# Kernel optimization log

Hardware: AMD Instinct MI355X
Metric: run time of the kernel (lower is better)

## Reference

```python
import jax, jax.numpy as jnp
import numpy as np

N = 50000
E = 800000
D_IN = 128
D_H = 128
D_OUT = 40
BN_EPS = 1e-5


def setup_inputs() -> dict:
    key = jax.random.key(0)
    ks = jax.random.split(key, 16)
    s = lambda d: 1.0 / np.sqrt(d)
    inp = {
        "x": jax.random.normal(ks[0], (N, D_IN), jnp.float32),
        "edge_index": jax.random.randint(ks[1], (2, E), 0, N, jnp.int64),
        # conv1 MLP: Linear(D_IN,D_H) -> BN -> ReLU -> Linear(D_H,D_H) -> ReLU
        "W1a": jax.random.uniform(ks[2], (D_IN, D_H), jnp.float32, -s(D_IN), s(D_IN)),
        "b1a": jnp.zeros((D_H,), jnp.float32),
        "g1": jnp.ones((D_H,), jnp.float32),
        "be1": jnp.zeros((D_H,), jnp.float32),
        "W2a": jax.random.uniform(ks[3], (D_H, D_H), jnp.float32, -s(D_H), s(D_H)),
        "b2a": jnp.zeros((D_H,), jnp.float32),
        # conv2 MLP
        "W1b": jax.random.uniform(ks[4], (D_H, D_H), jnp.float32, -s(D_H), s(D_H)),
        "b1b": jnp.zeros((D_H,), jnp.float32),
        "g2": jnp.ones((D_H,), jnp.float32),
        "be2": jnp.zeros((D_H,), jnp.float32),
        "W2b": jax.random.uniform(ks[5], (D_H, D_H), jnp.float32, -s(D_H), s(D_H)),
        "b2b": jnp.zeros((D_H,), jnp.float32),
        # head
        "Wl1": jax.random.uniform(ks[6], (D_H, D_H), jnp.float32, -s(D_H), s(D_H)),
        "bl1": jnp.zeros((D_H,), jnp.float32),
        "Wl2": jax.random.uniform(ks[7], (D_H, D_OUT), jnp.float32, -s(D_H), s(D_H)),
        "bl2": jnp.zeros((D_OUT,), jnp.float32),
    }
    return inp


def _batchnorm(h, gamma, beta):
    # BatchNorm1d in training mode: biased batch stats over the node dim
    mu = h.mean(axis=0)
    var = h.var(axis=0)
    return (h - mu) * jax.lax.rsqrt(var + BN_EPS) * gamma + beta


def _gin_conv(x, src, dst, W1, b1, gamma, beta, W2, b2):
    # sum-aggregation over neighbors (eps = 0): (1+eps)*x + sum_{j in N(i)} x_j
    agg = x + jax.ops.segment_sum(x[src], dst, num_segments=N)
    h = agg @ W1 + b1
    h = jax.nn.relu(_batchnorm(h, gamma, beta))
    return jax.nn.relu(h @ W2 + b2)


def reference(x, edge_index, W1a, b1a, g1, be1, W2a, b2a,
              W1b, b1b, g2, be2, W2b, b2b, Wl1, bl1, Wl2, bl2):
    src, dst = edge_index[0], edge_index[1]
    h = jax.nn.relu(_gin_conv(x, src, dst, W1a, b1a, g1, be1, W2a, b2a))
    # dropout is a no-op here (deterministic reference / eval)
    h = _gin_conv(h, src, dst, W1b, b1b, g2, be2, W2b, b2b)
    h = jax.nn.relu(h @ Wl1 + bl1)
    h = h @ Wl2 + bl2
    return jax.nn.log_softmax(h, axis=1)
```

## Files before the change

### kernel.cpp

```cpp
#include <hip/hip_runtime.h>
#include <math.h>

#define NN 50000
#define NE 800000
#define DD 128
#define DOUT 40
#define BN_EPS_F 1e-5f
#define BSTRIDE 32
#define OVF_MAX 8192
#define NPX (NN / 8)
#define EPB 1024
#define BUCKET_BLOCKS (((NE + EPB - 1) / EPB) * 8)
#define X2BF_BLOCKS 6250
#define WPREP_BLOCKS ((5 * 16384 + 255) / 256)
#define NSLOT 8
#define HST 136

typedef __attribute__((ext_vector_type(8))) short bf16x8;
typedef __attribute__((ext_vector_type(4))) float f32x4;

static __device__ __forceinline__ unsigned short f2bf(float f) {
  unsigned u = __float_as_uint(f);
  unsigned r = (u + 0x7FFFu + ((u >> 16) & 1u)) >> 16;
  return (unsigned short)r;
}
static __device__ __forceinline__ float bf2f(unsigned short u) {
  return __uint_as_float((unsigned)u << 16);
}

__global__ void k_zero(int* __restrict__ cnt, float* __restrict__ stats,
                       int* __restrict__ ovfc) {
  int i = blockIdx.x * 256 + threadIdx.x;
  if (i < NN) cnt[i] = 0;
  if (i < 2 * NSLOT * 2 * DD) stats[i] = 0.f;
  if (i == 0) ovfc[0] = 0;
}

__global__ void k_bucketprep(const int* __restrict__ srcI, const int* __restrict__ dstI,
                             int* __restrict__ cnt, unsigned short* __restrict__ bkt,
                             int* __restrict__ ovfc, unsigned* __restrict__ ovf,
                             const float4* __restrict__ x, ushort4* __restrict__ xb,
                             const float* __restrict__ W0, const float* __restrict__ W1,
                             const float* __restrict__ W2, const float* __restrict__ W3,
                             const float* __restrict__ W4, unsigned short* __restrict__ wf) {
  int b = blockIdx.x;
  if (b < BUCKET_BLOCKS) {
    int xcd = b & 7;
    int chunk = b >> 3;
    int lo = xcd * NPX, hi = lo + NPX;
    int e0 = chunk * EPB + threadIdx.x * 4;
    if (e0 < NE) {
      int4 d4 = *(const int4*)(dstI + e0);
      int4 s4 = *(const int4*)(srcI + e0);
      int dd[4] = {d4.x, d4.y, d4.z, d4.w};
      int ss[4] = {s4.x, s4.y, s4.z, s4.w};
#pragma unroll
      for (int i = 0; i < 4; i++) {
        int d = dd[i];
        if (d >= lo && d < hi) {
          int r = atomicAdd(&cnt[d], 1);
          if (r < BSTRIDE) {
            bkt[(size_t)d * BSTRIDE + r] = (unsigned short)ss[i];
          } else {
            int o = atomicAdd(ovfc, 1);
            if (o < OVF_MAX) ovf[o] = ((unsigned)d << 16) | (unsigned)ss[i];
          }
        }
      }
    }
  } else if (b < BUCKET_BLOCKS + X2BF_BLOCKS) {
    int i = (b - BUCKET_BLOCKS) * 256 + threadIdx.x;
    if (i < NN * 32) {
      float4 v = x[i];
      ushort4 r;
      r.x = f2bf(v.x); r.y = f2bf(v.y); r.z = f2bf(v.z); r.w = f2bf(v.w);
      xb[i] = r;
    }
  } else {
    int fid = (b - BUCKET_BLOCKS - X2BF_BLOCKS) * 256 + threadIdx.x;
    if (fid >= 5 * 16384) return;
    int g = fid >> 14;
    int r = fid & 16383;
    int i = r & 7;
    int lane = (r >> 3) & 63;
    int ks = (r >> 9) & 3;
    int ct = r >> 11;
    int k = ks * 32 + (lane >> 4) * 8 + i;
    int col = ct * 16 + (lane & 15);
    const float* Wp = (g == 0) ? W0 : (g == 1) ? W1 : (g == 2) ? W2 : (g == 3) ? W3 : W4;
    float w = Wp[k * DD + col];
    wf[g * 16384 + r] = f2bf(w);
  }
}

__global__ __launch_bounds__(512) void k_aggemm(
    const unsigned short* __restrict__ in, const int* __restrict__ cnt,
    const unsigned short* __restrict__ bkt,
    const int* __restrict__ ovfc, const unsigned* __restrict__ ovf,
    const unsigned short* __restrict__ wf, const float* __restrict__ bias,
    unsigned short* __restrict__ outB, float* __restrict__ statsOut) {
  __shared__ __align__(16) short lw[16384];
  __shared__ __align__(16) unsigned short hs[64 * HST];
  __shared__ float lbias[DD], ls[DD], lq[DD];
  int tid = threadIdx.x;
  int lane = tid & 63, wv = tid >> 6;
  int rbase = blockIdx.x * 64;

  {
    const float4* src = (const float4*)wf;
    float4* dst = (float4*)lw;
#pragma unroll
    for (int it = 0; it < 4; it++) dst[it * 512 + tid] = src[it * 512 + tid];
  }
  if (tid < DD) { lbias[tid] = bias[tid]; ls[tid] = 0.f; lq[tid] = 0.f; }

  {
    int l16 = tid & 15;
    const unsigned short* base = in + l16 * 8;
#pragma unroll
    for (int rep = 0; rep < 2; rep++) {
      int nl = (tid >> 4) + rep * 32;
      int node = rbase + nl;
      float a[8] = {0.f, 0.f, 0.f, 0.f, 0.f, 0.f, 0.f, 0.f};
      if (node < NN) {
        bf16x8 sv = *(const bf16x8*)(base + (size_t)node * DD);
#pragma unroll
        for (int i = 0; i < 8; i++) a[i] = bf2f((unsigned short)sv[i]);
        int cn = cnt[node];
        int ce = (cn < BSTRIDE) ? cn : BSTRIDE;
        const unsigned short* bp = bkt + (size_t)node * BSTRIDE;
        int j = 0;
        for (; j + 3 < ce; j += 4) {
          int s0 = bp[j], s1 = bp[j + 1], s2 = bp[j + 2], s3 = bp[j + 3];
          bf16x8 v0 = *(const bf16x8*)(base + (size_t)s0 * DD);
          bf16x8 v1 = *(const bf16x8*)(base + (size_t)s1 * DD);
          bf16x8 v2 = *(const bf16x8*)(base + (size_t)s2 * DD);
          bf16x8 v3 = *(const bf16x8*)(base + (size_t)s3 * DD);
#pragma unroll
          for (int i = 0; i < 8; i++)
            a[i] += bf2f((unsigned short)v0[i]) + bf2f((unsigned short)v1[i]) +
                    bf2f((unsigned short)v2[i]) + bf2f((unsigned short)v3[i]);
        }
        for (; j < ce; j++) {
          bf16x8 v0 = *(const bf16x8*)(base + (size_t)bp[j] * DD);
#pragma unroll
          for (int i = 0; i < 8; i++) a[i] += bf2f((unsigned short)v0[i]);
        }
        if (cn > BSTRIDE) {
          int no = ovfc[0];
          if (no > OVF_MAX) no = OVF_MAX;
          for (int o = 0; o < no; o++) {
            unsigned pr = ovf[o];
            if ((int)(pr >> 16) == node) {
              bf16x8 v0 = *(const bf16x8*)(base + (size_t)(pr & 0xFFFFu) * DD);
#pragma unroll
              for (int i = 0; i < 8; i++) a[i] += bf2f((unsigned short)v0[i]);
            }
          }
        }
      }
      bf16x8 hv;
#pragma unroll
      for (int i = 0; i < 8; i++) hv[i] = (short)f2bf(a[i]);
      *(bf16x8*)(&hs[nl * HST + l16 * 8]) = hv;
    }
  }
  __syncthreads();

  int rblk = wv >> 1, ch = wv & 1;
  int kq = (lane >> 4) * 8;
  bf16x8 araw[4];
  {
    int lr = rblk * 16 + (lane & 15);
#pragma unroll
    for (int ks = 0; ks < 4; ks++)
      araw[ks] = *(const bf16x8*)(&hs[lr * HST + ks * 32 + kq]);
  }
  f32x4 acc[4];
#pragma unroll
  for (int ct = 0; ct < 4; ct++) acc[ct] = (f32x4){0.f, 0.f, 0.f, 0.f};
  const bf16x8* lwv = (const bf16x8*)lw;
#pragma unroll
  for (int ks = 0; ks < 4; ks++) {
#pragma unroll
    for (int ct = 0; ct < 4; ct++) {
      bf16x8 bh = lwv[((ch * 4 + ct) * 4 + ks) * 64 + lane];
      acc[ct] = __builtin_amdgcn_mfma_f32_16x16x32_bf16(araw[ks], bh, acc[ct], 0, 0, 0);
    }
  }

  {
    int r0 = rbase + rblk * 16 + (lane >> 4) * 4;
#pragma unroll
    for (int ct = 0; ct < 4; ct++) {
      int col = ch * 64 + ct * 16 + (lane & 15);
      float bb = lbias[col];
      float s = 0.f, q = 0.f;
#pragma unroll
      for (int j = 0; j < 4; j++) {
        int row = r0 + j;
        if (row < NN) {
          float v = acc[ct][j] + bb;
          outB[(size_t)row * DD + col] = f2bf(v);
          s += v; q += v * v;
        }
      }
      s += __shfl_xor(s, 16); s += __shfl_xor(s, 32);
      q += __shfl_xor(q, 16); q += __shfl_xor(q, 32);
      if ((lane >> 4) == 0) {
        atomicAdd(&ls[col], s);
        atomicAdd(&lq[col], q);
      }
    }
  }
  __syncthreads();
  if (tid < DD) {
    float* slot = statsOut + (blockIdx.x & (NSLOT - 1)) * 2 * DD;
    atomicAdd(&slot[tid], ls[tid]);
    atomicAdd(&slot[DD + tid], lq[tid]);
  }
}

template<bool BN_IN, bool RELU_OUT, bool STATS_OUT, bool HEAD>
__global__ __launch_bounds__(512) void k_mgemm(
    const unsigned short* __restrict__ in, const unsigned short* __restrict__ wf,
    const float* __restrict__ bias, float* __restrict__ outF,
    unsigned short* __restrict__ outB,
    const float* __restrict__ statsIn, float* __restrict__ statsOut,
    const float* __restrict__ gamma, const float* __restrict__ beta,
    const float* __restrict__ W2h, const float* __restrict__ b2h) {
  constexpr int SMEM_BYTES = HEAD ? 54272 : 32768;
  __shared__ __align__(16) char smem[SMEM_BYTES];
  __shared__ float scs[DD], shs[DD], lbias[DD], ls[DD], lq[DD];
  short* lw = (short*)smem;
  int tid = threadIdx.x;
  int lane = tid & 63, wv = tid >> 6;
  int rbase = blockIdx.x * 128 + wv * 16;
  int kq = (lane >> 4) * 8;

  bf16x8 araw[4];
  {
    int row = rbase + (lane & 15);
    bool v = row < NN;
    const unsigned short* ap = in + (size_t)row * DD + kq;
    bf16x8 zz = {0, 0, 0, 0, 0, 0, 0, 0};
#pragma unroll
    for (int ks = 0; ks < 4; ks++)
      araw[ks] = v ? *(const bf16x8*)(ap + ks * 32) : zz;
  }

  {
    const float4* src = (const float4*)wf;
    float4* dst = (float4*)lw;
#pragma unroll
    for (int it = 0; it < 4; it++) dst[it * 512 + tid] = src[it * 512 + tid];
  }
  if (tid < DD) {
    lbias[tid] = bias[tid];
    if (STATS_OUT) { ls[tid] = 0.f; lq[tid] = 0.f; }
    if (BN_IN) {
      float su = 0.f, sq = 0.f;
#pragma unroll
      for (int s = 0; s < NSLOT; s++) {
        su += statsIn[s * 2 * DD + tid];
        sq += statsIn[s * 2 * DD + DD + tid];
      }
      float mu  = su * (1.0f / NN);
      float var = sq * (1.0f / NN) - mu * mu;
      float sc  = gamma[tid] * rsqrtf(var + BN_EPS_F);
      scs[tid] = sc;
      shs[tid] = beta[tid] - mu * sc;
    }
  }
  __syncthreads();

  bf16x8 ahi[4];
  if constexpr (BN_IN) {
#pragma unroll
    for (int ks = 0; ks < 4; ks++) {
      const float4* s4 = (const float4*)&scs[ks * 32 + kq];
      const float4* h4 = (const float4*)&shs[ks * 32 + kq];
      float4 sa = s4[0], sb = s4[1], ha = h4[0], hb = h4[1];
      float ss[8] = {sa.x, sa.y, sa.z, sa.w, sb.x, sb.y, sb.z, sb.w};
      float hh[8] = {ha.x, ha.y, ha.z, ha.w, hb.x, hb.y, hb.z, hb.w};
      bf16x8 h;
#pragma unroll
      for (int i = 0; i < 8; i++) {
        float xv = fmaxf(bf2f((unsigned short)araw[ks][i]) * ss[i] + hh[i], 0.f);
        h[i] = (short)f2bf(xv);
      }
      ahi[ks] = h;
    }
  } else {
#pragma unroll
    for (int ks = 0; ks < 4; ks++) ahi[ks] = araw[ks];
  }

  f32x4 acc[8];
#pragma unroll
  for (int ct = 0; ct < 8; ct++) acc[ct] = (f32x4){0.f, 0.f, 0.f, 0.f};
  const bf16x8* lwv = (const bf16x8*)lw;
#pragma unroll
  for (int ks = 0; ks < 4; ks++) {
#pragma unroll
    for (int ct = 0; ct < 8; ct++) {
      bf16x8 bh = lwv[(ct * 4 + ks) * 64 + lane];
      acc[ct] = __builtin_amdgcn_mfma_f32_16x16x32_bf16(ahi[ks], bh, acc[ct], 0, 0, 0);
    }
  }

  if constexpr (!HEAD) {
    int r0 = rbase + (lane >> 4) * 4;
#pragma unroll
    for (int ct = 0; ct < 8; ct++) {
      int col = ct * 16 + (lane & 15);
      float bb = lbias[col];
      float s = 0.f, q = 0.f;
#pragma unroll
      for (int j = 0; j < 4; j++) {
        int row = r0 + j;
        if (row < NN) {
          float v = acc[ct][j] + bb;
          if (RELU_OUT) v = fmaxf(v, 0.f);
          outB[(size_t)row * DD + col] = f2bf(v);
          if (STATS_OUT) { s += v; q += v * v; }
        }
      }
      if (STATS_OUT) {
        s += __shfl_xor(s, 16); s += __shfl_xor(s, 32);
        q += __shfl_xor(q, 16); q += __shfl_xor(q, 32);
        if ((lane >> 4) == 0) {
          atomicAdd(&ls[col], s);
          atomicAdd(&lq[col], q);
        }
      }
    }
    if (STATS_OUT) {
      __syncthreads();
      if (tid < DD) {
        float* slot = statsOut + (blockIdx.x & (NSLOT - 1)) * 2 * DD;
        atomicAdd(&slot[tid], ls[tid]);
        atomicAdd(&slot[DD + tid], lq[tid]);
      }
    }
  } else {
    unsigned short* hs2 = (unsigned short*)smem;
    float* W2s = (float*)(smem + 33792);
    __syncthreads();
    {
      int lr0 = wv * 16 + (lane >> 4) * 4;
#pragma unroll
      for (int ct = 0; ct < 8; ct++) {
        int col = ct * 16 + (lane & 15);
        float bb = lbias[col];
#pragma unroll
        for (int j = 0; j < 4; j++) {
          float v = fmaxf(acc[ct][j] + bb, 0.f);
          hs2[(lr0 + j) * 132 + col] = f2bf(v);
        }
      }
      const float4* W2g = (const float4*)W2h;
      float4* W2s4 = (float4*)W2s;
#pragma unroll
      for (int it = 0; it < 3; it++) {
        int idx = it * 512 + tid;
        if (idx < 1280) W2s4[idx] = W2g[idx];
      }
    }
    __syncthreads();
    int lrow = tid >> 2, q = tid & 3;
    int grow = blockIdx.x * 128 + lrow;
    float a2[40];
#pragma unroll
    for (int j = 0; j < 40; j++) a2[j] = 0.f;
    for (int kk = 0; kk < 32; kk++) {
      int k = kk * 4 + q;
      float hv = bf2f(hs2[lrow * 132 + k]);
      const float4* wrow = (const float4*)(W2s + k * DOUT);
#pragma unroll
      for (int j4 = 0; j4 < 10; j4++) {
        float4 w = wrow[j4];
        a2[j4 * 4 + 0] += hv * w.x;
        a2[j4 * 4 + 1] += hv * w.y;
        a2[j4 * 4 + 2] += hv * w.z;
        a2[j4 * 4 + 3] += hv * w.w;
      }
    }
#pragma unroll
    for (int j = 0; j < 40; j++) {
      a2[j] += __shfl_xor(a2[j], 1);
      a2[j] += __shfl_xor(a2[j], 2);
    }
    if (q == 0 && grow < NN) {
      const float4* b24 = (const float4*)b2h;
      float m = -INFINITY;
#pragma unroll
      for (int j4 = 0; j4 < 10; j4++) {
        float4 bb = b24[j4];
        a2[j4 * 4 + 0] += bb.x; a2[j4 * 4 + 1] += bb.y;
        a2[j4 * 4 + 2] += bb.z; a2[j4 * 4 + 3] += bb.w;
      }
#pragma unroll
      for (int j = 0; j < 40; j++) m = fmaxf(m, a2[j]);
      float s = 0.f;
#pragma unroll
      for (int j = 0; j < 40; j++) s += expf(a2[j] - m);
      float d = m + logf(s);
      float4* out4 = (float4*)(outF + (size_t)grow * DOUT);
#pragma unroll
      for (int j4 = 0; j4 < 10; j4++) {
        float4 v = make_float4(a2[j4 * 4 + 0] - d, a2[j4 * 4 + 1] - d,
                               a2[j4 * 4 + 2] - d, a2[j4 * 4 + 3] - d);
        out4[j4] = v;
      }
    }
  }
}

extern "C" void kernel_launch(void* const* d_in, const int* in_sizes, int n_in,
                              void* d_out, int out_size, void* d_ws, size_t ws_size,
                              hipStream_t stream) {
  const float* x   = (const float*)d_in[0];
  const int*   ei  = (const int*)d_in[1];
  const float* W1a = (const float*)d_in[2];
  const float* b1a = (const float*)d_in[3];
  const float* g1  = (const float*)d_in[4];
  const float* be1 = (const float*)d_in[5];
  const float* W2a = (const float*)d_in[6];
  const float* b2a = (const float*)d_in[7];
  const float* W1b = (const float*)d_in[8];
  const float* b1b = (const float*)d_in[9];
  const float* g2  = (const float*)d_in[10];
  const float* be2 = (const float*)d_in[11];
  const float* W2b = (const float*)d_in[12];
  const float* b2b = (const float*)d_in[13];
  const float* Wl1 = (const float*)d_in[14];
  const float* bl1 = (const float*)d_in[15];
  const float* Wl2 = (const float*)d_in[16];
  const float* bl2 = (const float*)d_in[17];
  float* out = (float*)d_out;

  unsigned short* bufX = (unsigned short*)d_ws;
  unsigned short* bufA = bufX + (size_t)NN * DD;
  unsigned short* bufB = bufA + (size_t)NN * DD;
  float* stats1 = (float*)(bufB + (size_t)NN * DD);
  float* stats2 = stats1 + NSLOT * 2 * DD;
  int*   cnt    = (int*)(stats2 + NSLOT * 2 * DD);
  int*   ovfc   = cnt + NN;
  unsigned* ovf = (unsigned*)(ovfc + 4);
  unsigned short* bkt = (unsigned short*)(ovf + OVF_MAX);
  size_t wfOff = (((size_t)(bkt + (size_t)NN * BSTRIDE) - (size_t)d_ws) + 15) & ~(size_t)15;
  unsigned short* wfrag = (unsigned short*)((char*)d_ws + wfOff);

  const int* srcI = ei;
  const int* dstI = ei + NE;

  dim3 blk(256);
  int gemmGrid = (NN + 127) / 128;
  int agGrid   = (NN + 63) / 64;
  int bpGrid   = BUCKET_BLOCKS + X2BF_BLOCKS + WPREP_BLOCKS;
  int zeroGrid = (NN + 255) / 256;

  k_zero<<<zeroGrid, blk, 0, stream>>>(cnt, stats1, ovfc);
  k_bucketprep<<<bpGrid, blk, 0, stream>>>(srcI, dstI, cnt, bkt, ovfc, ovf,
                                           (const float4*)x, (ushort4*)bufX,
                                           W1a, W2a, W1b, W2b, Wl1, wfrag);

  k_aggemm<<<agGrid, 512, 0, stream>>>(bufX, cnt, bkt, ovfc, ovf,
                                       wfrag + 0 * 16384, b1a, bufB, stats1);
  k_mgemm<true, true, false, false><<<gemmGrid, 512, 0, stream>>>(
      bufB, wfrag + 1 * 16384, b2a, nullptr, bufA,
      stats1, nullptr, g1, be1, nullptr, nullptr);
  k_aggemm<<<agGrid, 512, 0, stream>>>(bufA, cnt, bkt, ovfc, ovf,
                                       wfrag + 2 * 16384, b1b, bufB, stats2);
  k_mgemm<true, true, false, false><<<gemmGrid, 512, 0, stream>>>(
      bufB, wfrag + 3 * 16384, b2b, nullptr, bufA,
      stats2, nullptr, g2, be2, nullptr, nullptr);
  k_mgemm<false, false, false, true><<<gemmGrid, 512, 0, stream>>>(
      bufA, wfrag + 4 * 16384, bl1, out, nullptr,
      nullptr, nullptr, nullptr, nullptr, Wl2, bl2);
}
```

Measured before the change: 192.4 us.

## Fuse second-conv output GEMM with head GEMMs into one tail kernel

Merges the conv2 second linear layer (BN+ReLU input, ReLU output) with the head Linear+ReLU+Linear+log_softmax into a single kernel. The intermediate activation stays in LDS (XOR-swizzled layout) instead of going to global memory, which removes one kernel launch and one full activation write/read. The non-head GEMM is specialized into a non-template kernel. The fused kernel uses more shared memory per block, which may reduce occupancy.

```diff
diff --git a/kernel.cpp b/kernel.cpp
--- a/kernel.cpp
+++ b/kernel.cpp
@@ -221,17 +221,13 @@
   }
 }
 
-template<bool BN_IN, bool RELU_OUT, bool STATS_OUT, bool HEAD>
-__global__ __launch_bounds__(512) void k_mgemm(
+__global__ __launch_bounds__(512) void k_mgemm2(
     const unsigned short* __restrict__ in, const unsigned short* __restrict__ wf,
-    const float* __restrict__ bias, float* __restrict__ outF,
-    unsigned short* __restrict__ outB,
-    const float* __restrict__ statsIn, float* __restrict__ statsOut,
-    const float* __restrict__ gamma, const float* __restrict__ beta,
-    const float* __restrict__ W2h, const float* __restrict__ b2h) {
-  constexpr int SMEM_BYTES = HEAD ? 54272 : 32768;
-  __shared__ __align__(16) char smem[SMEM_BYTES];
-  __shared__ float scs[DD], shs[DD], lbias[DD], ls[DD], lq[DD];
+    const float* __restrict__ bias, unsigned short* __restrict__ outB,
+    const float* __restrict__ statsIn,
+    const float* __restrict__ gamma, const float* __restrict__ beta) {
+  __shared__ __align__(16) char smem[32768];
+  __shared__ float scs[DD], shs[DD], lbias[DD];
   short* lw = (short*)smem;
   int tid = threadIdx.x;
   int lane = tid & 63, wv = tid >> 6;
@@ -248,7 +244,6 @@
     for (int ks = 0; ks < 4; ks++)
       araw[ks] = v ? *(const bf16x8*)(ap + ks * 32) : zz;
   }
-
   {
     const float4* src = (const float4*)wf;
     float4* dst = (float4*)lw;
@@ -257,43 +252,35 @@
   }
   if (tid < DD) {
     lbias[tid] = bias[tid];
-    if (STATS_OUT) { ls[tid] = 0.f; lq[tid] = 0.f; }
-    if (BN_IN) {
-      float su = 0.f, sq = 0.f;
-#pragma unroll
-      for (int s = 0; s < NSLOT; s++) {
-        su += statsIn[s * 2 * DD + tid];
-        sq += statsIn[s * 2 * DD + DD + tid];
-      }
-      float mu  = su * (1.0f / NN);
-      float var = sq * (1.0f / NN) - mu * mu;
-      float sc  = gamma[tid] * rsqrtf(var + BN_EPS_F);
-      scs[tid] = sc;
-      shs[tid] = beta[tid] - mu * sc;
-    }
+    float su = 0.f, sq = 0.f;
+#pragma unroll
+    for (int s = 0; s < NSLOT; s++) {
+      su += statsIn[s * 2 * DD + tid];
+      sq += statsIn[s * 2 * DD + DD + tid];
+    }
+    float mu  = su * (1.0f / NN);
+    float var = sq * (1.0f / NN) - mu * mu;
+    float sc  = gamma[tid] * rsqrtf(var + BN_EPS_F);
+    scs[tid] = sc;
+    shs[tid] = beta[tid] - mu * sc;
   }
   __syncthreads();
 
   bf16x8 ahi[4];
-  if constexpr (BN_IN) {
-#pragma unroll
-    for (int ks = 0; ks < 4; ks++) {
-      const float4* s4 = (const float4*)&scs[ks * 32 + kq];
-      const float4* h4 = (const float4*)&shs[ks * 32 + kq];
-      float4 sa = s4[0], sb = s4[1], ha = h4[0], hb = h4[1];
-      float ss[8] = {sa.x, sa.y, sa.z, sa.w, sb.x, sb.y, sb.z, sb.w};
-      float hh[8] = {ha.x, ha.y, ha.z, ha.w, hb.x, hb.y, hb.z, hb.w};
-      bf16x8 h;
-#pragma unroll
-      for (int i = 0; i < 8; i++) {
-        float xv = fmaxf(bf2f((unsigned short)araw[ks][i]) * ss[i] + hh[i], 0.f);
-        h[i] = (short)f2bf(xv);
-      }
-      ahi[ks] = h;
-    }
-  } else {
-#pragma unroll
-    for (int ks = 0; ks < 4; ks++) ahi[ks] = araw[ks];
+#pragma unroll
+  for (int ks = 0; ks < 4; ks++) {
+    const float4* s4 = (const float4*)&scs[ks * 32 + kq];
+    const float4* h4 = (const float4*)&shs[ks * 32 + kq];
+    float4 sa = s4[0], sb = s4[1], ha = h4[0], hb = h4[1];
+    float ss[8] = {sa.x, sa.y, sa.z, sa.w, sb.x, sb.y, sb.z, sb.w};
+    float hh[8] = {ha.x, ha.y, ha.z, ha.w, hb.x, hb.y, hb.z, hb.w};
+    bf16x8 h;
+#pragma unroll
+    for (int i = 0; i < 8; i++) {
+      float xv = fmaxf(bf2f((unsigned short)araw[ks][i]) * ss[i] + hh[i], 0.f);
+      h[i] = (short)f2bf(xv);
+    }
+    ahi[ks] = h;
   }
 
   f32x4 acc[8];
@@ -309,110 +296,222 @@
     }
   }
 
-  if constexpr (!HEAD) {
-    int r0 = rbase + (lane >> 4) * 4;
+  int r0 = rbase + (lane >> 4) * 4;
+#pragma unroll
+  for (int ct = 0; ct < 8; ct++) {
+    int col = ct * 16 + (lane & 15);
+    float bb = lbias[col];
+#pragma unroll
+    for (int j = 0; j < 4; j++) {
+      int row = r0 + j;
+      if (row < NN) {
+        float v = fmaxf(acc[ct][j] + bb, 0.f);
+        outB[(size_t)row * DD + col] = f2bf(v);
+      }
+    }
+  }
+}
+
+__global__ __launch_bounds__(512) void k_tail2(
+    const unsigned short* __restrict__ in, const unsigned short* __restrict__ wfA,
+    const float* __restrict__ biasA, const float* __restrict__ statsIn,
+    const float* __restrict__ gamma, const float* __restrict__ beta,
+    const unsigned short* __restrict__ wfB, const float* __restrict__ biasB,
+    const float* __restrict__ W2h, const float* __restrict__ b2h,
+    float* __restrict__ outF) {
+  __shared__ __align__(16) char R1[32768];
+  __shared__ __align__(16) char R2[32768];
+  __shared__ float scs[DD], shs[DD], lbA[DD], lbB[DD];
+  int tid = threadIdx.x;
+  int lane = tid & 63, wv = tid >> 6;
+  int rbase = blockIdx.x * 128 + wv * 16;
+  int kq = (lane >> 4) * 8;
+
+  bf16x8 araw[4];
+  {
+    int row = rbase + (lane & 15);
+    bool v = row < NN;
+    const unsigned short* ap = in + (size_t)row * DD + kq;
+    bf16x8 zz = {0, 0, 0, 0, 0, 0, 0, 0};
+#pragma unroll
+    for (int ks = 0; ks < 4; ks++)
+      araw[ks] = v ? *(const bf16x8*)(ap + ks * 32) : zz;
+  }
+  {
+    const float4* s1 = (const float4*)wfA;
+    const float4* s2 = (const float4*)wfB;
+    float4* d1 = (float4*)R1;
+    float4* d2 = (float4*)R2;
+#pragma unroll
+    for (int it = 0; it < 4; it++) {
+      d1[it * 512 + tid] = s1[it * 512 + tid];
+      d2[it * 512 + tid] = s2[it * 512 + tid];
+    }
+  }
+  if (tid < DD) {
+    lbA[tid] = biasA[tid];
+    lbB[tid] = biasB[tid];
+    float su = 0.f, sq = 0.f;
+#pragma unroll
+    for (int s = 0; s < NSLOT; s++) {
+      su += statsIn[s * 2 * DD + tid];
+      sq += statsIn[s * 2 * DD + DD + tid];
+    }
+    float mu  = su * (1.0f / NN);
+    float var = sq * (1.0f / NN) - mu * mu;
+    float sc  = gamma[tid] * rsqrtf(var + BN_EPS_F);
+    scs[tid] = sc;
+    shs[tid] = beta[tid] - mu * sc;
+  }
+  __syncthreads();
+
+  bf16x8 ahi[4];
+#pragma unroll
+  for (int ks = 0; ks < 4; ks++) {
+    const float4* s4 = (const float4*)&scs[ks * 32 + kq];
+    const float4* h4 = (const float4*)&shs[ks * 32 + kq];
+    float4 sa = s4[0], sb = s4[1], ha = h4[0], hb = h4[1];
+    float ss[8] = {sa.x, sa.y, sa.z, sa.w, sb.x, sb.y, sb.z, sb.w};
+    float hh[8] = {ha.x, ha.y, ha.z, ha.w, hb.x, hb.y, hb.z, hb.w};
+    bf16x8 h;
+#pragma unroll
+    for (int i = 0; i < 8; i++) {
+      float xv = fmaxf(bf2f((unsigned short)araw[ks][i]) * ss[i] + hh[i], 0.f);
+      h[i] = (short)f2bf(xv);
+    }
+    ahi[ks] = h;
+  }
+
+  f32x4 acc[8];
+#pragma unroll
+  for (int ct = 0; ct < 8; ct++) acc[ct] = (f32x4){0.f, 0.f, 0.f, 0.f};
+  {
+    const bf16x8* l1 = (const bf16x8*)R1;
+#pragma unroll
+    for (int ks = 0; ks < 4; ks++) {
+#pragma unroll
+      for (int ct = 0; ct < 8; ct++) {
+        bf16x8 bh = l1[(ct * 4 + ks) * 64 + lane];
+        acc[ct] = __builtin_amdgcn_mfma_f32_16x16x32_bf16(ahi[ks], bh, acc[ct], 0, 0, 0);
+      }
+    }
+  }
+  __syncthreads();
+
+  {
+    int fr0 = (lane >> 4) * 4;
+    int lr0 = wv * 16 + fr0;
 #pragma unroll
     for (int ct = 0; ct < 8; ct++) {
       int col = ct * 16 + (lane & 15);
-      float bb = lbias[col];
-      float s = 0.f, q = 0.f;
+      float bb = lbA[col];
 #pragma unroll
       for (int j = 0; j < 4; j++) {
-        int row = r0 + j;
-        if (row < NN) {
-          float v = acc[ct][j] + bb;
-          if (RELU_OUT) v = fmaxf(v, 0.f);
-          outB[(size_t)row * DD + col] = f2bf(v);
-          if (STATS_OUT) { s += v; q += v * v; }
-        }
-      }
-      if (STATS_OUT) {
-        s += __shfl_xor(s, 16); s += __shfl_xor(s, 32);
-        q += __shfl_xor(q, 16); q += __shfl_xor(q, 32);
-        if ((lane >> 4) == 0) {
-          atomicAdd(&ls[col], s);
-          atomicAdd(&lq[col], q);
-        }
-      }
-    }
-    if (STATS_OUT) {
-      __syncthreads();
-      if (tid < DD) {
-        float* slot = statsOut + (blockIdx.x & (NSLOT - 1)) * 2 * DD;
-        atomicAdd(&slot[tid], ls[tid]);
-        atomicAdd(&slot[DD + tid], lq[tid]);
-      }
-    }
-  } else {
-    unsigned short* hs2 = (unsigned short*)smem;
-    float* W2s = (float*)(smem + 33792);
-    __syncthreads();
-    {
-      int lr0 = wv * 16 + (lane >> 4) * 4;
+        int r = lr0 + j;
+        float v = fmaxf(acc[ct][j] + bb, 0.f);
+        int byt = (r * 256 + col * 2) ^ ((r & 7) << 4);
+        *(unsigned short*)(R1 + byt) = f2bf(v);
+      }
+    }
+  }
+  __syncthreads();
+
+  bf16x8 a2[4];
+  {
+    int lr = wv * 16 + (lane & 15);
+#pragma unroll
+    for (int ks = 0; ks < 4; ks++) {
+      int byt = (lr * 256 + ks * 64 + kq * 2) ^ ((lr & 7) << 4);
+      a2[ks] = *(const bf16x8*)(R1 + byt);
+    }
+  }
+  f32x4 ac3[8];
+#pragma unroll
+  for (int ct = 0; ct < 8; ct++) ac3[ct] = (f32x4){0.f, 0.f, 0.f, 0.f};
+  {
+    const bf16x8* l2 = (const bf16x8*)R2;
+#pragma unroll
+    for (int ks = 0; ks < 4; ks++) {
 #pragma unroll
       for (int ct = 0; ct < 8; ct++) {
-        int col = ct * 16 + (lane & 15);
-        float bb = lbias[col];
-#pragma unroll
-        for (int j = 0; j < 4; j++) {
-          float v = fmaxf(acc[ct][j] + bb, 0.f);
-          hs2[(lr0 + j) * 132 + col] = f2bf(v);
-        }
-      }
-      const float4* W2g = (const float4*)W2h;
-      float4* W2s4 = (float4*)W2s;
-#pragma unroll
-      for (int it = 0; it < 3; it++) {
-        int idx = it * 512 + tid;
-        if (idx < 1280) W2s4[idx] = W2g[idx];
-      }
-    }
-    __syncthreads();
-    int lrow = tid >> 2, q = tid & 3;
-    int grow = blockIdx.x * 128 + lrow;
-    float a2[40];
-#pragma unroll
-    for (int j = 0; j < 40; j++) a2[j] = 0.f;
-    for (int kk = 0; kk < 32; kk++) {
-      int k = kk * 4 + q;
-      float hv = bf2f(hs2[lrow * 132 + k]);
-      const float4* wrow = (const float4*)(W2s + k * DOUT);
-#pragma unroll
-      for (int j4 = 0; j4 < 10; j4++) {
-        float4 w = wrow[j4];
-        a2[j4 * 4 + 0] += hv * w.x;
-        a2[j4 * 4 + 1] += hv * w.y;
-        a2[j4 * 4 + 2] += hv * w.z;
-        a2[j4 * 4 + 3] += hv * w.w;
-      }
-    }
-#pragma unroll
-    for (int j = 0; j < 40; j++) {
-      a2[j] += __shfl_xor(a2[j], 1);
-      a2[j] += __shfl_xor(a2[j], 2);
-    }
-    if (q == 0 && grow < NN) {
-      const float4* b24 = (const float4*)b2h;
-      float m = -INFINITY;
-#pragma unroll
-      for (int j4 = 0; j4 < 10; j4++) {
-        float4 bb = b24[j4];
-        a2[j4 * 4 + 0] += bb.x; a2[j4 * 4 + 1] += bb.y;
-        a2[j4 * 4 + 2] += bb.z; a2[j4 * 4 + 3] += bb.w;
-      }
-#pragma unroll
-      for (int j = 0; j < 40; j++) m = fmaxf(m, a2[j]);
-      float s = 0.f;
-#pragma unroll
-      for (int j = 0; j < 40; j++) s += expf(a2[j] - m);
-      float d = m + logf(s);
-      float4* out4 = (float4*)(outF + (size_t)grow * DOUT);
-#pragma unroll
-      for (int j4 = 0; j4 < 10; j4++) {
-        float4 v = make_float4(a2[j4 * 4 + 0] - d, a2[j4 * 4 + 1] - d,
-                               a2[j4 * 4 + 2] - d, a2[j4 * 4 + 3] - d);
-        out4[j4] = v;
-      }
+        bf16x8 bh = l2[(ct * 4 + ks) * 64 + lane];
+        ac3[ct] = __builtin_amdgcn_mfma_f32_16x16x32_bf16(a2[ks], bh, ac3[ct], 0, 0, 0);
+      }
+    }
+  }
+  __syncthreads();
+
+  {
+    int fr0 = (lane >> 4) * 4;
+    int lr0 = wv * 16 + fr0;
+#pragma unroll
+    for (int ct = 0; ct < 8; ct++) {
+      int col = ct * 16 + (lane & 15);
+      float bb = lbB[col];
+#pragma unroll
+      for (int j = 0; j < 4; j++) {
+        int r = lr0 + j;
+        float v = fmaxf(ac3[ct][j] + bb, 0.f);
+        int byt = (r * 256 + col * 2) ^ ((r & 7) << 4);
+        *(unsigned short*)(R1 + byt) = f2bf(v);
+      }
+    }
+    const float4* W2g = (const float4*)W2h;
+    float4* W2s4 = (float4*)R2;
+#pragma unroll
+    for (int it = 0; it < 3; it++) {
+      int idx = it * 512 + tid;
+      if (idx < 1280) W2s4[idx] = W2g[idx];
+    }
+  }
+  __syncthreads();
+
+  int lrow = tid >> 2, q = tid & 3;
+  int grow = blockIdx.x * 128 + lrow;
+  const float* W2s = (const float*)R2;
+  float av[40];
+#pragma unroll
+  for (int j = 0; j < 40; j++) av[j] = 0.f;
+  for (int kk = 0; kk < 32; kk++) {
+    int k = kk * 4 + q;
+    int byt = (lrow * 256 + k * 2) ^ ((lrow & 7) << 4);
+    float hv = bf2f(*(const unsigned short*)(R1 + byt));
+    const float4* wrow = (const float4*)(W2s + k * DOUT);
+#pragma unroll
+    for (int j4 = 0; j4 < 10; j4++) {
+      float4 w = wrow[j4];
+      av[j4 * 4 + 0] += hv * w.x;
+      av[j4 * 4 + 1] += hv * w.y;
+      av[j4 * 4 + 2] += hv * w.z;
+      av[j4 * 4 + 3] += hv * w.w;
+    }
+  }
+#pragma unroll
+  for (int j = 0; j < 40; j++) {
+    av[j] += __shfl_xor(av[j], 1);
+    av[j] += __shfl_xor(av[j], 2);
+  }
+  if (q == 0 && grow < NN) {
+    const float4* b24 = (const float4*)b2h;
+    float m = -INFINITY;
+#pragma unroll
+    for (int j4 = 0; j4 < 10; j4++) {
+      float4 bb = b24[j4];
+      av[j4 * 4 + 0] += bb.x; av[j4 * 4 + 1] += bb.y;
+      av[j4 * 4 + 2] += bb.z; av[j4 * 4 + 3] += bb.w;
+    }
+#pragma unroll
+    for (int j = 0; j < 40; j++) m = fmaxf(m, av[j]);
+    float s = 0.f;
+#pragma unroll
+    for (int j = 0; j < 40; j++) s += expf(av[j] - m);
+    float d = m + logf(s);
+    float4* out4 = (float4*)(outF + (size_t)grow * DOUT);
+#pragma unroll
+    for (int j4 = 0; j4 < 10; j4++) {
+      float4 v = make_float4(av[j4 * 4 + 0] - d, av[j4 * 4 + 1] - d,
+                             av[j4 * 4 + 2] - d, av[j4 * 4 + 3] - d);
+      out4[j4] = v;
     }
   }
 }
@@ -468,15 +567,11 @@
 
   k_aggemm<<<agGrid, 512, 0, stream>>>(bufX, cnt, bkt, ovfc, ovf,
                                        wfrag + 0 * 16384, b1a, bufB, stats1);
-  k_mgemm<true, true, false, false><<<gemmGrid, 512, 0, stream>>>(
-      bufB, wfrag + 1 * 16384, b2a, nullptr, bufA,
-      stats1, nullptr, g1, be1, nullptr, nullptr);
+  k_mgemm2<<<gemmGrid, 512, 0, stream>>>(bufB, wfrag + 1 * 16384, b2a, bufA,
+                                         stats1, g1, be1);
   k_aggemm<<<agGrid, 512, 0, stream>>>(bufA, cnt, bkt, ovfc, ovf,
                                        wfrag + 2 * 16384, b1b, bufB, stats2);
-  k_mgemm<true, true, false, false><<<gemmGrid, 512, 0, stream>>>(
-      bufB, wfrag + 3 * 16384, b2b, nullptr, bufA,
-      stats2, nullptr, g2, be2, nullptr, nullptr);
-  k_mgemm<false, false, false, true><<<gemmGrid, 512, 0, stream>>>(
-      bufA, wfrag + 4 * 16384, bl1, out, nullptr,
-      nullptr, nullptr, nullptr, nullptr, Wl2, bl2);
-}
+  k_tail2<<<gemmGrid, 512, 0, stream>>>(bufB, wfrag + 3 * 16384, b2b,
+                                        stats2, g2, be2,
+                                        wfrag + 4 * 16384, bl1, Wl2, bl2, out);
+}
```

After: 181.8 us. 5.5% less time.
